# Optimization experiments

Hardware: AMD Instinct MI355X
Metric: run time of the kernel (lower is better)

The kernel has to match this reference:

```python
import jax, jax.numpy as jnp
import numpy as np

# Device / mapping constants from the source (is_low_resistance=True branch)
V_REF = 0.25
G_MIN = 0.1
G_MAX = 1.0
K_V = 2.0 * V_REF  # x_to_V scale
N_AVG = 2.18
N_STD = 0.115


def setup_inputs() -> dict:
    key = jax.random.key(0)
    k_x, k_wp, k_wn, k_n = jax.random.split(key, 4)
    n_in, n_out, batch = 1024, 512, 128
    stdv = 1.0 / np.sqrt(n_in)
    x = jax.random.uniform(k_x, (batch, n_in), dtype=jnp.float32)
    w_pos = 0.5 + stdv * jax.random.normal(k_wp, (n_in, n_out), dtype=jnp.float32)
    w_neg = 0.5 + stdv * jax.random.normal(k_wn, (n_in, n_out), dtype=jnp.float32)
    b_pos = 0.5 * jnp.ones((n_out,), jnp.float32)
    b_neg = 0.5 * jnp.ones((n_out,), jnp.float32)
    # per-device I-V nonlinearity parameter n ~ N(n_avg, n_std), one per crossbar cell
    n_param = N_AVG + N_STD * jax.random.normal(k_n, (n_in + 1, 2 * n_out), dtype=jnp.float32)
    return {"x": x, "w_pos": w_pos, "w_neg": w_neg, "b_pos": b_pos, "b_neg": b_neg,
            "n_param": n_param}


def _memristor_dense(x, w_pos, w_neg, b_pos, b_neg, n_param):
    x = jnp.clip(x, 0.0, 1.0)
    # append bias rows, interleave pos/neg along output axis -> (n_in+1, 2*n_out)
    cw_pos = jnp.concatenate([w_pos, b_pos[None, :]], axis=0)
    cw_neg = jnp.concatenate([w_neg, b_neg[None, :]], axis=0)
    w = jnp.stack([cw_pos, cw_neg], axis=-1).reshape(cw_pos.shape[0], -1)
    # append ones column to inputs (bias voltage line)
    inp = jnp.concatenate([x, jnp.ones((x.shape[0], 1), x.dtype)], axis=1)  # (B, n_in+1)
    # weight -> effective conductance (differential scheme), then offset by G_min
    max_w = jnp.max(jnp.abs(w))
    k_G = (G_MAX - G_MIN) / max_w
    G = jnp.abs(k_G * w) + G_MIN  # (n_in+1, 2*n_out)
    # input -> voltage
    V = K_V * inp  # (B, n_in+1)
    # nonlinear-parameter I-V model: I = sign(V) * G * V_ref * (|V|/V_ref) ** (log2(n) + 1)
    # (satisfies n = I(2*V_ref) / (2 * I(V_ref)))
    exponent = jnp.log2(n_param) + 1.0  # (n_in+1, 2*n_out)
    v_ratio = jnp.abs(V) / V_REF  # (B, n_in+1)
    vr = v_ratio[:, :, None]  # (B, n_in+1, 1)
    vr_safe = jnp.where(vr > 0, vr, 1.0)
    pow_term = jnp.where(vr > 0, vr_safe ** exponent[None, :, :], 0.0)  # (B, n_in+1, 2*n_out)
    I_ind = jnp.sign(V)[:, :, None] * (G * V_REF)[None, :, :] * pow_term
    # sum currents along bit lines
    I = jnp.sum(I_ind, axis=1)  # (B, 2*n_out)
    # currents -> outputs (differential pairs are interleaved)
    y = (I[:, 0::2] - I[:, 1::2]) / (K_V * k_G)  # (B, n_out)
    return y


def reference(x, w_pos, w_neg, b_pos, b_neg, n_param):
    return _memristor_dense(x, w_pos, w_neg, b_pos, b_neg, n_param)
```

## Files before the change

kernel.cpp:

```cpp
#include <hip/hip_runtime.h>
#include <hip/hip_bf16.h>


#define LOG2F(v)  __builtin_amdgcn_logf(v)
#define EXP2F(v)  __builtin_amdgcn_exp2f(v)

#define BB 16
#define BJ 16
#define KI 128
#define LROW (KI + 4)

__global__ __launch_bounds__(256) void maxw_kernel(
    const float* __restrict__ w_pos, const float* __restrict__ w_neg,
    const float* __restrict__ b_pos, const float* __restrict__ b_neg,
    int n_w, int n_b, float* __restrict__ ws) {
  float m = 0.0f;
  int tid = blockIdx.x * blockDim.x + threadIdx.x;
  int stride = gridDim.x * blockDim.x;
  for (int i = tid; i < n_w; i += stride) {
    m = fmaxf(m, fabsf(w_pos[i]));
    m = fmaxf(m, fabsf(w_neg[i]));
  }
  if (tid < n_b) {
    m = fmaxf(m, fabsf(b_pos[tid]));
    m = fmaxf(m, fabsf(b_neg[tid]));
  }
  #pragma unroll
  for (int off = 32; off > 0; off >>= 1)
    m = fmaxf(m, __shfl_down(m, off, 64));
  __shared__ float sm[4];
  int lane = threadIdx.x & 63, wv = threadIdx.x >> 6;
  if (lane == 0) sm[wv] = m;
  __syncthreads();
  if (threadIdx.x == 0) {
    m = fmaxf(fmaxf(sm[0], sm[1]), fmaxf(sm[2], sm[3]));
    atomicMax((int*)ws, __float_as_int(m));
  }
}

__global__ __launch_bounds__(256) void memristor_kernel(
    const float* __restrict__ x, const float* __restrict__ w_pos,
    const float* __restrict__ w_neg, const float* __restrict__ b_pos,
    const float* __restrict__ b_neg, const float* __restrict__ n_param,
    const float* __restrict__ ws, float* __restrict__ y) {
  __shared__ float sL[BB * LROW];
  __shared__ float sA0[BJ * LROW];
  __shared__ float sA1[BJ * LROW];
  __shared__ float sE0[BJ * LROW];
  __shared__ float sE1[BJ * LROW];

  const float max_w = ws[0];
  const float c0 = max_w * (0.05f / 0.9f);

  const int j0 = blockIdx.x * BJ;
  const int b0 = blockIdx.y * BB;
  const int zt = blockIdx.z;
  const int t  = threadIdx.x;
  const int jj = t & 15;
  const int bb = t >> 4;
  float accP = 0.0f, accN = 0.0f;

  const float2* np2 = (const float2*)n_param;

  for (int c = zt * 4; c < zt * 4 + 4; ++c) {
    const int i0 = c * KI;
    #pragma unroll
    for (int r = 0; r < (BB * KI) / 256; ++r) {
      int idx = r * 256 + t;
      int k  = idx & (KI - 1);
      int bl = idx >> 7;
      float v = x[(b0 + bl) * 1024 + i0 + k];
      v = fminf(fmaxf(v, 0.0f), 1.0f);
      sL[bl * LROW + k] = LOG2F(2.0f * v);
    }
    #pragma unroll
    for (int r = 0; r < (BJ * KI) / 256; ++r) {
      int idx = r * 256 + t;
      int jl = idx & (BJ - 1);
      int il = idx >> 4;
      int gi = i0 + il;
      float wp = w_pos[gi * 512 + j0 + jl];
      float wn = w_neg[gi * 512 + j0 + jl];
      float2 np = np2[gi * 512 + j0 + jl];
      sA0[jl * LROW + il] = fmaf(0.5f, fabsf(wp), c0);
      sA1[jl * LROW + il] = fmaf(0.5f, fabsf(wn), c0);
      sE0[jl * LROW + il] = LOG2F(np.x) + 1.0f;
      sE1[jl * LROW + il] = LOG2F(np.y) + 1.0f;
    }
    __syncthreads();
    const float* pL  = &sL[bb * LROW];
    const float* pA0 = &sA0[jj * LROW];
    const float* pA1 = &sA1[jj * LROW];
    const float* pE0 = &sE0[jj * LROW];
    const float* pE1 = &sE1[jj * LROW];
    #pragma unroll 4
    for (int k = 0; k < KI; ++k) {
      float l  = pL[k];
      float t0 = EXP2F(pE0[k] * l);
      float t1 = EXP2F(pE1[k] * l);
      accP = fmaf(pA0[k], t0, accP);
      accN = fmaf(pA1[k], t1, accN);
    }
    __syncthreads();
  }

  if (zt == 1) {
    int jg = j0 + jj;
    float2 np = np2[1024 * 512 + jg];
    float a0 = fmaf(0.5f, fabsf(b_pos[jg]), c0);
    float a1 = fmaf(0.5f, fabsf(b_neg[jg]), c0);
    accP = fmaf(a0, EXP2F(LOG2F(np.x) + 1.0f), accP);
    accN = fmaf(a1, EXP2F(LOG2F(np.y) + 1.0f), accN);
  }

  atomicAdd(&y[(b0 + bb) * 512 + (j0 + jj)], accP - accN);
}

extern "C" void kernel_launch(void* const* d_in, const int* in_sizes, int n_in,
                              void* d_out, int out_size, void* d_ws, size_t ws_size,
                              hipStream_t stream) {
  const float* x       = (const float*)d_in[0];
  const float* w_pos   = (const float*)d_in[1];
  const float* w_neg   = (const float*)d_in[2];
  const float* b_pos   = (const float*)d_in[3];
  const float* b_neg   = (const float*)d_in[4];
  const float* n_param = (const float*)d_in[5];
  float* y   = (float*)d_out;
  float* wsf = (float*)d_ws;

  (void)hipMemsetAsync(d_ws, 0, 4, stream);
  (void)hipMemsetAsync(d_out, 0, (size_t)out_size * 4, stream);

  maxw_kernel<<<dim3(256), dim3(256), 0, stream>>>(
      w_pos, w_neg, b_pos, b_neg, in_sizes[1], in_sizes[3], wsf);

  memristor_kernel<<<dim3(32, 8, 2), dim3(256), 0, stream>>>(
      x, w_pos, w_neg, b_pos, b_neg, n_param, wsf, y);
}
```

Before: 103.9 us.

## Fuse memsets into setup kernel, split K four ways, pack params into float4

Replaces the two memsets and the atomicMax reduction with one setup kernel. That kernel zeroes the output, computes per-block partial max values with float4 loads, and writes them to workspace, where the main kernel reduces them. The main kernel now splits the reduction dimension four ways instead of two (1024 blocks, KI=64) for more parallelism. It also packs A0/E0/A1/E1 into one float4 shared array so the inner loop needs fewer LDS loads. The cost is more atomicAdds on the output, and every block must reread 32 workspace values.

```diff
diff --git a/kernel.cpp b/kernel.cpp
--- a/kernel.cpp
+++ b/kernel.cpp
@@ -5,37 +5,46 @@
 #define LOG2F(v)  __builtin_amdgcn_logf(v)
 #define EXP2F(v)  __builtin_amdgcn_exp2f(v)
 
-#define BB 16
-#define BJ 16
-#define KI 128
-#define LROW (KI + 4)
+#define NJ 16
+#define NB 16
+#define KI 64
+#define KROW4 65
+#define LROW 68
 
-__global__ __launch_bounds__(256) void maxw_kernel(
+#define NPART 32
+
+__global__ __launch_bounds__(256) void setup_kernel(
     const float* __restrict__ w_pos, const float* __restrict__ w_neg,
     const float* __restrict__ b_pos, const float* __restrict__ b_neg,
-    int n_w, int n_b, float* __restrict__ ws) {
+    float* __restrict__ y, float* __restrict__ ws) {
+  const int t = threadIdx.x, blk = blockIdx.x;
+  float4 z4 = make_float4(0.f, 0.f, 0.f, 0.f);
+  float4* y4 = (float4*)y;
+  y4[blk * 512 + t]       = z4;
+  y4[blk * 512 + 256 + t] = z4;
+  const float4* wp4 = (const float4*)w_pos;
+  const float4* wn4 = (const float4*)w_neg;
   float m = 0.0f;
-  int tid = blockIdx.x * blockDim.x + threadIdx.x;
-  int stride = gridDim.x * blockDim.x;
-  for (int i = tid; i < n_w; i += stride) {
-    m = fmaxf(m, fabsf(w_pos[i]));
-    m = fmaxf(m, fabsf(w_neg[i]));
+  #pragma unroll 4
+  for (int r = 0; r < 16; ++r) {
+    int i = blk * 4096 + r * 256 + t;
+    float4 a = wp4[i], b = wn4[i];
+    m = fmaxf(m, fmaxf(fmaxf(fabsf(a.x), fabsf(a.y)), fmaxf(fabsf(a.z), fabsf(a.w))));
+    m = fmaxf(m, fmaxf(fmaxf(fabsf(b.x), fabsf(b.y)), fmaxf(fabsf(b.z), fabsf(b.w))));
   }
-  if (tid < n_b) {
-    m = fmaxf(m, fabsf(b_pos[tid]));
-    m = fmaxf(m, fabsf(b_neg[tid]));
+  if (blk == 0) {
+    m = fmaxf(m, fmaxf(fabsf(b_pos[t]), fabsf(b_pos[t + 256])));
+    m = fmaxf(m, fmaxf(fabsf(b_neg[t]), fabsf(b_neg[t + 256])));
   }
   #pragma unroll
   for (int off = 32; off > 0; off >>= 1)
     m = fmaxf(m, __shfl_down(m, off, 64));
   __shared__ float sm[4];
-  int lane = threadIdx.x & 63, wv = threadIdx.x >> 6;
+  int lane = t & 63, wv = t >> 6;
   if (lane == 0) sm[wv] = m;
   __syncthreads();
-  if (threadIdx.x == 0) {
-    m = fmaxf(fmaxf(sm[0], sm[1]), fmaxf(sm[2], sm[3]));
-    atomicMax((int*)ws, __float_as_int(m));
-  }
+  if (t == 0)
+    ws[blk] = fmaxf(fmaxf(sm[0], sm[1]), fmaxf(sm[2], sm[3]));
 }
 
 __global__ __launch_bounds__(256) void memristor_kernel(
@@ -43,17 +52,16 @@
     const float* __restrict__ w_neg, const float* __restrict__ b_pos,
     const float* __restrict__ b_neg, const float* __restrict__ n_param,
     const float* __restrict__ ws, float* __restrict__ y) {
-  __shared__ float sL[BB * LROW];
-  __shared__ float sA0[BJ * LROW];
-  __shared__ float sA1[BJ * LROW];
-  __shared__ float sE0[BJ * LROW];
-  __shared__ float sE1[BJ * LROW];
+  __shared__ float4 sP[NJ * KROW4];
+  __shared__ float  sL[NB * LROW];
 
-  const float max_w = ws[0];
-  const float c0 = max_w * (0.05f / 0.9f);
+  float mw = 0.0f;
+  #pragma unroll
+  for (int i = 0; i < NPART; ++i) mw = fmaxf(mw, ws[i]);
+  const float c0 = mw * (0.05f / 0.9f);
 
-  const int j0 = blockIdx.x * BJ;
-  const int b0 = blockIdx.y * BB;
+  const int j0 = blockIdx.x * NJ;
+  const int b0 = blockIdx.y * NB;
   const int zt = blockIdx.z;
   const int t  = threadIdx.x;
   const int jj = t & 15;
@@ -62,49 +70,44 @@
 
   const float2* np2 = (const float2*)n_param;
 
-  for (int c = zt * 4; c < zt * 4 + 4; ++c) {
-    const int i0 = c * KI;
+  for (int c = 0; c < 4; ++c) {
+    const int i0 = zt * 256 + c * KI;
     #pragma unroll
-    for (int r = 0; r < (BB * KI) / 256; ++r) {
+    for (int r = 0; r < (NB * KI) / 256; ++r) {
       int idx = r * 256 + t;
       int k  = idx & (KI - 1);
-      int bl = idx >> 7;
+      int bl = idx >> 6;
       float v = x[(b0 + bl) * 1024 + i0 + k];
       v = fminf(fmaxf(v, 0.0f), 1.0f);
       sL[bl * LROW + k] = LOG2F(2.0f * v);
     }
     #pragma unroll
-    for (int r = 0; r < (BJ * KI) / 256; ++r) {
+    for (int r = 0; r < (NJ * KI) / 256; ++r) {
       int idx = r * 256 + t;
-      int jl = idx & (BJ - 1);
+      int jl = idx & (NJ - 1);
       int il = idx >> 4;
       int gi = i0 + il;
       float wp = w_pos[gi * 512 + j0 + jl];
       float wn = w_neg[gi * 512 + j0 + jl];
       float2 np = np2[gi * 512 + j0 + jl];
-      sA0[jl * LROW + il] = fmaf(0.5f, fabsf(wp), c0);
-      sA1[jl * LROW + il] = fmaf(0.5f, fabsf(wn), c0);
-      sE0[jl * LROW + il] = LOG2F(np.x) + 1.0f;
-      sE1[jl * LROW + il] = LOG2F(np.y) + 1.0f;
+      sP[jl * KROW4 + il] = make_float4(
+          fmaf(0.5f, fabsf(wp), c0), LOG2F(np.x) + 1.0f,
+          fmaf(0.5f, fabsf(wn), c0), LOG2F(np.y) + 1.0f);
     }
     __syncthreads();
-    const float* pL  = &sL[bb * LROW];
-    const float* pA0 = &sA0[jj * LROW];
-    const float* pA1 = &sA1[jj * LROW];
-    const float* pE0 = &sE0[jj * LROW];
-    const float* pE1 = &sE1[jj * LROW];
-    #pragma unroll 4
+    const float4* pP = &sP[jj * KROW4];
+    const float*  pL = &sL[bb * LROW];
+    #pragma unroll 8
     for (int k = 0; k < KI; ++k) {
+      float4 p = pP[k];
       float l  = pL[k];
-      float t0 = EXP2F(pE0[k] * l);
-      float t1 = EXP2F(pE1[k] * l);
-      accP = fmaf(pA0[k], t0, accP);
-      accN = fmaf(pA1[k], t1, accN);
+      accP = fmaf(p.x, EXP2F(p.y * l), accP);
+      accN = fmaf(p.z, EXP2F(p.w * l), accN);
     }
     __syncthreads();
   }
 
-  if (zt == 1) {
+  if (zt == 3) {
     int jg = j0 + jj;
     float2 np = np2[1024 * 512 + jg];
     float a0 = fmaf(0.5f, fabsf(b_pos[jg]), c0);
@@ -128,12 +131,9 @@
   float* y   = (float*)d_out;
   float* wsf = (float*)d_ws;
 
-  (void)hipMemsetAsync(d_ws, 0, 4, stream);
-  (void)hipMemsetAsync(d_out, 0, (size_t)out_size * 4, stream);
+  setup_kernel<<<dim3(NPART), dim3(256), 0, stream>>>(
+      w_pos, w_neg, b_pos, b_neg, y, wsf);
 
-  maxw_kernel<<<dim3(256), dim3(256), 0, stream>>>(
-      w_pos, w_neg, b_pos, b_neg, in_sizes[1], in_sizes[3], wsf);
-
-  memristor_kernel<<<dim3(32, 8, 2), dim3(256), 0, stream>>>(
+  memristor_kernel<<<dim3(32, 8, 4), dim3(256), 0, stream>>>(
       x, w_pos, w_neg, b_pos, b_neg, n_param, wsf, y);
 }
```

Result: faster. 93.82 us (-9.7%).
